# Kernel optimization log

Measured on AMD Instinct MI355X. Metric: run time of the kernel, lower is better.

Reference implementation:

```python
import jax, jax.numpy as jnp
import numpy as np

BS, L, D = 2048, 32, 768
KS = 5  # gaussian kernel size
EPS = 1e-5


def layer_norm(x, g, b):
    m = x.mean(-1, keepdims=True)
    var = ((x - m) ** 2).mean(-1, keepdims=True)
    return (x - m) * jax.lax.rsqrt(var + EPS) * g + b


def setup_inputs() -> dict:
    key = jax.random.key(0)
    ks = jax.random.split(key, 12)
    s = 0.02
    return {
        "v": jax.random.normal(ks[0], (BS, L, D), jnp.float32),
        "qa": jax.random.normal(ks[1], (BS, D), jnp.float32),
        # v_proj: LayerNorm -> Linear(D,D) -> GELU
        "vp_lng": jnp.ones((D,), jnp.float32),
        "vp_lnb": jnp.zeros((D,), jnp.float32),
        "vp_w": jax.random.normal(ks[2], (D, D), jnp.float32) * s,
        "vp_b": jnp.zeros((D,), jnp.float32),
        # qa_proj: LayerNorm -> Linear(D,D) -> GELU
        "qp_lng": jnp.ones((D,), jnp.float32),
        "qp_lnb": jnp.zeros((D,), jnp.float32),
        "qp_w": jax.random.normal(ks[3], (D, D), jnp.float32) * s,
        "qp_b": jnp.zeros((D,), jnp.float32),
        # grounding: LayerNorm -> Linear(D,D/2) -> GELU -> Linear(D/2,1) -> Softmax(dim=-2)
        "g_lng": jnp.ones((D,), jnp.float32),
        "g_lnb": jnp.zeros((D,), jnp.float32),
        "g_w1": jax.random.normal(ks[4], (D, D // 2), jnp.float32) * s,
        "g_b1": jnp.zeros((D // 2,), jnp.float32),
        "g_w2": jax.random.normal(ks[5], (D // 2, 1), jnp.float32) * s,
        "g_b2": jnp.zeros((1,), jnp.float32),
        # adaptive gaussian filter sigma (scalar parameter, initial 1.0)
        "sigma": jnp.array(1.0, jnp.float32),
    }


def reference(v, qa, vp_lng, vp_lnb, vp_w, vp_b, qp_lng, qp_lnb, qp_w, qp_b,
              g_lng, g_lnb, g_w1, g_b1, g_w2, g_b2, sigma):
    bs, length = v.shape[0], v.shape[1]
    # projections (exact erf GELU, matching torch nn.GELU default)
    v_p = jax.nn.gelu(layer_norm(v, vp_lng, vp_lnb) @ vp_w + vp_b, approximate=False)
    qa_p = jax.nn.gelu(layer_norm(qa, qp_lng, qp_lnb) @ qp_w + qp_b, approximate=False)
    # gate = tanh(v @ qa) : [bs, L, 1]
    gate = jnp.tanh(jnp.einsum('bld,bd->bl', v_p, qa_p))[..., None]
    # grounding head -> softmax over frames
    h = layer_norm(v_p * gate, g_lng, g_lnb)
    h = jax.nn.gelu(h @ g_w1 + g_b1, approximate=False)
    logits = h @ g_w2 + g_b2                      # [bs, L, 1]
    ori_key = jax.nn.softmax(logits, axis=1)[..., 0]  # [bs, L]
    # adaptive gaussian smoothing (depthwise conv1d, symmetric 5-tap kernel) + softmax
    xk = jnp.arange(KS, dtype=jnp.float32) - KS // 2
    kern = jnp.exp(-0.5 * (xk / sigma) ** 2)
    kern = kern / kern.sum()
    xp = jnp.pad(ori_key, ((0, 0), (KS // 2, KS // 2)))
    taps = jnp.stack([xp[:, k:k + length] for k in range(KS)], axis=0)  # [KS, bs, L]
    smoothed = jnp.einsum('k,kbl->bl', kern, taps)
    key_gs = jax.nn.softmax(smoothed, axis=1)         # [bs, L]
    # find_best_interval_v2, vectorized: among windows of size {1,3,5} that
    # contain the (first) argmax frame, pick the window with highest prob-sum;
    # ties resolve to smallest window then earliest start (strict > in loop ==
    # first occurrence of the max in (w, start) order == jnp.argmax semantics).
    pmax = jnp.argmax(key_gs, axis=1)                 # [bs]
    cum = jnp.pad(jnp.cumsum(key_gs, axis=1), ((0, 0), (1, 0)))
    scores_all, starts_all, ends_all = [], [], []
    for w in (1, 3, 5):
        s = jnp.arange(length - w + 1)
        sums = cum[:, s + w] - cum[:, s]              # sliding window sums
        contains = (pmax[:, None] >= s[None, :]) & (pmax[:, None] < s[None, :] + w)
        scores_all.append(jnp.where(contains, sums, -jnp.inf))
        starts_all.append(s)
        ends_all.append(s + w)                        # NOTE: exclusive end stored, as in original
    scores = jnp.concatenate(scores_all, axis=1)
    starts = jnp.concatenate(starts_all)
    ends = jnp.concatenate(ends_all)
    idx = jnp.argmax(scores, axis=1)
    st = starts[idx]
    en = ends[idx]
    max_indices = jnp.stack([st, en], axis=1)         # [bs, 2]
    rng = jnp.arange(length)
    mask = (rng[None, :] >= st[:, None]) & (rng[None, :] <= en[:, None])
    start_time = st.astype(jnp.float32) / 31.0
    end_time = en.astype(jnp.float32) / 31.0
    return key_gs, max_indices, start_time, end_time, mask, ori_key
```

## Files before the change

### kernel.cpp

```cpp
#include <hip/hip_runtime.h>
#include <math.h>
#include <stdint.h>


#define DEV __device__ __forceinline__

typedef __attribute__((ext_vector_type(8))) short short8v;
typedef __attribute__((ext_vector_type(4))) float f32x4;
typedef __attribute__((ext_vector_type(4))) uint32_t u32x4;

constexpr int KDIM  = 768;
constexpr int CHUNK = 32768;

constexpr int OFF_KG   = 0;
constexpr int OFF_MI   = 65536;
constexpr int OFF_ST   = 69632;
constexpr int OFF_ET   = 71680;
constexpr int OFF_MASK = 73728;
constexpr int OFF_ORI  = 139264;

DEV float wave_sum(float v) { for (int o = 32; o; o >>= 1) v += __shfl_xor(v, o); return v; }
DEV float wave_max(float v) { for (int o = 32; o; o >>= 1) v = fmaxf(v, __shfl_xor(v, o)); return v; }

DEV float gelu_fast(float x) {
    float z = x * 0.70710678118654752f;
    float s = fabsf(z);
    float t = __builtin_amdgcn_rcpf(fmaf(0.3275911f, s, 1.0f));
    float p = t * fmaf(t, fmaf(t, fmaf(t, fmaf(t, 1.061405429f, -1.453152027f),
                                       1.421413741f), -0.284496736f), 0.254829592f);
    float e = __expf(-s * s);
    float er = copysignf(1.0f - p * e, z);
    return 0.5f * x * (1.0f + er);
}

DEV short f2bf(float x) {
    uint32_t u = __builtin_bit_cast(uint32_t, x);
    u = u + 0x7fffu + ((u >> 16) & 1u);
    return (short)(u >> 16);
}
DEV float bf2f(short b) {
    uint32_t u = ((uint32_t)(uint16_t)b) << 16;
    return __builtin_bit_cast(float, u);
}
DEV float asf(uint32_t u) { return __builtin_bit_cast(float, u); }

DEV uint32_t packhl(float x) {
    uint32_t u  = __builtin_bit_cast(uint32_t, x);
    uint32_t hb = u & 0xffff0000u;
    float rem   = x - asf(hb);
    return hb | (uint32_t)(uint16_t)f2bf(rem);
}

DEV void gl_lds16(const void* g, void* l) {
    __builtin_amdgcn_global_load_lds(
        (const __attribute__((address_space(1))) uint32_t*)g,
        (__attribute__((address_space(3))) uint32_t*)l, 16, 0, 0);
}

DEV void unpack8(u32x4 p0, u32x4 p1, short8v& hi, short8v& lo) {
    u32x4 h, l;
    h.x = (p0.x >> 16) | (p0.y & 0xffff0000u);
    h.y = (p0.z >> 16) | (p0.w & 0xffff0000u);
    h.z = (p1.x >> 16) | (p1.y & 0xffff0000u);
    h.w = (p1.z >> 16) | (p1.w & 0xffff0000u);
    l.x = (p0.x & 0xffffu) | (p0.y << 16);
    l.y = (p0.z & 0xffffu) | (p0.w << 16);
    l.z = (p1.x & 0xffffu) | (p1.y << 16);
    l.w = (p1.z & 0xffffu) | (p1.w << 16);
    hi = __builtin_bit_cast(short8v, h);
    lo = __builtin_bit_cast(short8v, l);
}

__global__ __launch_bounds__(256)
void prep_A1(const float* __restrict__ X, const float* __restrict__ g,
             const float* __restrict__ b, short* __restrict__ Ah, short* __restrict__ Al)
{
    int w = threadIdx.x >> 6, lane = threadIdx.x & 63;
    int row = blockIdx.x * 4 + w;
    const float4* xr = (const float4*)(X + (size_t)row * KDIM);
    float4 xv[3]; float s = 0.f, ss = 0.f;
#pragma unroll
    for (int i = 0; i < 3; ++i) {
        xv[i] = xr[lane + i * 64];
        s  += xv[i].x + xv[i].y + xv[i].z + xv[i].w;
        ss += xv[i].x * xv[i].x + xv[i].y * xv[i].y + xv[i].z * xv[i].z + xv[i].w * xv[i].w;
    }
    s = wave_sum(s); ss = wave_sum(ss);
    float m = s * (1.f / 768.f), var = ss * (1.f / 768.f) - m * m;
    float sa = rsqrtf(var + 1e-5f), ta = -m * sa;
#pragma unroll
    for (int i = 0; i < 3; ++i) {
        int idx = lane + i * 64;
        float4 gv = ((const float4*)g)[idx];
        float4 bv = ((const float4*)b)[idx];
        float a0 = fmaf(fmaf(xv[i].x, sa, ta), gv.x, bv.x);
        float a1 = fmaf(fmaf(xv[i].y, sa, ta), gv.y, bv.y);
        float a2 = fmaf(fmaf(xv[i].z, sa, ta), gv.z, bv.z);
        float a3 = fmaf(fmaf(xv[i].w, sa, ta), gv.w, bv.w);
        short h0 = f2bf(a0), h1 = f2bf(a1), h2 = f2bf(a2), h3 = f2bf(a3);
        ushort4 hv, lv;
        hv.x = (uint16_t)h0; hv.y = (uint16_t)h1; hv.z = (uint16_t)h2; hv.w = (uint16_t)h3;
        lv.x = (uint16_t)f2bf(a0 - bf2f(h0)); lv.y = (uint16_t)f2bf(a1 - bf2f(h1));
        lv.z = (uint16_t)f2bf(a2 - bf2f(h2)); lv.w = (uint16_t)f2bf(a3 - bf2f(h3));
        ((ushort4*)(Ah + (size_t)row * KDIM))[idx] = hv;
        ((ushort4*)(Al + (size_t)row * KDIM))[idx] = lv;
    }
}

__global__ __launch_bounds__(256)
void prep_W(const float* __restrict__ W, const float* __restrict__ scale,
            short* __restrict__ Bh, short* __restrict__ Bl, int N)
{
    __shared__ float t[32][33];
    int bx = blockIdx.x, by = blockIdx.y;
    int lx = threadIdx.x & 31, ly = threadIdx.x >> 5;
#pragma unroll
    for (int r = 0; r < 32; r += 8)
        t[ly + r][lx] = W[(size_t)(by * 32 + ly + r) * N + bx * 32 + lx];
    __syncthreads();
    float sc = scale ? scale[by * 32 + lx] : 1.0f;
#pragma unroll
    for (int r = 0; r < 32; r += 8) {
        float v = t[lx][ly + r] * sc;
        short hi = f2bf(v);
        size_t o = (size_t)(bx * 32 + ly + r) * KDIM + by * 32 + lx;
        Bh[o] = hi;
        Bl[o] = f2bf(v - bf2f(hi));
    }
}

__global__ __launch_bounds__(256)
void colsums(const float* __restrict__ W1, const float* __restrict__ g2,
             const float* __restrict__ lb2, const float* __restrict__ b1,
             float* __restrict__ c1, float* __restrict__ c2)
{
    int w = threadIdx.x >> 6, lane = threadIdx.x & 63;
    int n = blockIdx.x * 4 + w;
    float s1 = 0.f, s2 = 0.f;
    for (int k = lane; k < 768; k += 64) {
        float wv = W1[(size_t)k * 384 + n];
        s1 += g2[k] * wv;
        s2 += lb2[k] * wv;
    }
    s1 = wave_sum(s1); s2 = wave_sum(s2);
    if (lane == 0) { c1[n] = s1; c2[n] = b1[n] + s2; }
}

__global__ __launch_bounds__(256)
void stats2(const float* __restrict__ sums, float2* __restrict__ st2, int chunk_off)
{
    int r = chunk_off + blockIdx.x * 256 + threadIdx.x;
    float s = 0.f, ss = 0.f, d = 0.f;
#pragma unroll
    for (int p = 0; p < 8; ++p) {
        s  += sums[(size_t)(0 * 8 + p) * 65536 + r];
        ss += sums[(size_t)(1 * 8 + p) * 65536 + r];
        d  += sums[(size_t)(2 * 8 + p) * 65536 + r];
    }
    float gate = tanhf(d);
    float m = s * (1.f / 768.f), var = ss * (1.f / 768.f) - m * m;
    float den = rsqrtf(gate * gate * var + 1e-5f);
    st2[r] = make_float2(gate * den, -gate * m * den);
}

#define VMW(N_) asm volatile("s_waitcnt vmcnt(" #N_ ")" ::: "memory")
#define SCB __builtin_amdgcn_sched_barrier(0)

#define STG(U_, KT_, KS_) gl_lds16(sp[U_] + (size_t)(KT_) * (KS_),            \
    lds + (((KT_) & 1) ? BUFSZ : 0) + (U_) * 4096 + toff)

#define STGALL(KT_) do {                                                      \
    STG(0, KT_, KSTA); STG(1, KT_, KSTA); STG(2, KT_, KSTA);                  \
    STG(3, KT_, KSTA); STG(4, KT_, 64); STG(5, KT_, 64); STG(6, KT_, 64);     \
    STG(7, KT_, 64); STG(8, KT_, 64); STG(9, KT_, 64); } while (0)

#define RDA(dst, BOFF) do { _Pragma("unroll")                                 \
    for (int mf = 0; mf < 4; ++mf) {                                          \
        int rA = wm * 64 + mf * 16 + lr;                                      \
        dst[mf] = *(const short8v*)(bb + (BOFF) + rA * 64 +                   \
                                    ((lh ^ ((rA >> 1) & 3)) << 4));           \
    } } while (0)

#define RDA2 do { RDA(ah, 0); RDA(al, 8192); } while (0)

#define RDAP do { _Pragma("unroll")                                           \
    for (int mf = 0; mf < 4; ++mf) {                                          \
        int rA = wm * 64 + mf * 16 + lr;                                      \
        const char* pr = bb + rA * 128;                                       \
        int x_ = rA & 7;                                                      \
        u32x4 p0 = *(const u32x4*)(pr + (((2 * lh) ^ x_) << 4));              \
        u32x4 p1 = *(const u32x4*)(pr + (((2 * lh + 1) ^ x_) << 4));          \
        unpack8(p0, p1, ah[mf], al[mf]);                                      \
    } } while (0)

#define RDB(dst, BOFF) do { _Pragma("unroll")                                 \
    for (int nf = 0; nf < 6; ++nf) {                                          \
        int rB = wn * 96 + nf * 16 + lr;                                      \
        dst[nf] = *(const short8v*)(bb + (BOFF) + rB * 64 +                   \
                                    ((lh ^ ((rB >> 1) & 3)) << 4));           \
    } } while (0)

#define BODY(KT_, NL_, ARD) do {                                              \
    if (NL_) { STGALL((KT_) + 1); }                                           \
    SCB;                                                                      \
    if (NL_) { VMW(10); } else { VMW(0); }                                    \
    SCB;                                                                      \
    __builtin_amdgcn_s_barrier();                \
    const char* bb = lds + (((KT_) & 1) ? BUFSZ : 0);                         \
    ARD; RDB(bh, 16384); RDB(bl, 28672);                                      \
    asm volatile("s_waitcnt lgkmcnt(0)" ::: "memory");                        \
    SCB;                                                                      \
    __builtin_amdgcn_s_barrier();                     \
    __builtin_amdgcn_s_setprio(1);                                            \
    _Pragma("unroll")                                                         \
    for (int mf = 0; mf < 4; ++mf)                                            \
        _Pragma("unroll")                                                     \
        for (int nf = 0; nf < 6; ++nf) {                                      \
            acc[mf][nf] = __builtin_amdgcn_mfma_f32_16x16x32_bf16(            \
                ah[mf], bh[nf], acc[mf][nf], 0, 0, 0);                        \
            acc[mf][nf] = __builtin_amdgcn_mfma_f32_16x16x32_bf16(            \
                ah[mf], bl[nf], acc[mf][nf], 0, 0, 0);                        \
            acc[mf][nf] = __builtin_amdgcn_mfma_f32_16x16x32_bf16(            \
                al[mf], bh[nf], acc[mf][nf], 0, 0, 0);                        \
        }                                                                     \
    __builtin_amdgcn_s_setprio(0);                                            \
    SCB;                                                                      \
} while (0)

template<int MODE>
__global__ __launch_bounds__(256, 2)
void gemm8(const short* __restrict__ Ah_g, const short* __restrict__ Al_g,
           const uint32_t* __restrict__ Ap_g,
           const short* __restrict__ Bh_g, const short* __restrict__ Bl_g,
           const float* __restrict__ bias, uint32_t* __restrict__ O_hl,
           const float* __restrict__ qa_p, float* __restrict__ sums,
           const float2* __restrict__ st2, const float* __restrict__ c1,
           const float* __restrict__ c2, const float* __restrict__ w2,
           float* __restrict__ partials, int chunk_off)
{
    constexpr int BUFSZ = 40960;
    constexpr int KSTA  = (MODE == 0) ? 64 : 128;
    extern __shared__ __align__(16) char lds[];

    const int t = threadIdx.x;
    const int w = t >> 6, lane = t & 63;
    const int lr = lane & 15, lh = lane >> 4;
    const int wm = w >> 1, wn = w & 1;

    const int gx = gridDim.x, nwg = gx * gridDim.y;
    int bidx = blockIdx.y * gx + blockIdx.x;
    int wid = (bidx & 7) * (nwg >> 3) + (bidx >> 3);
    const int bx = wid % gx, by = wid / gx;
    const int row0 = by * 128, col0 = bx * 192;

    const int r_ = t >> 2, c_ = t & 3;
    const int swz_ = (c_ ^ ((r_ >> 1) & 3)) << 3;
    const int rA_ = t >> 3, cA_ = t & 7;
    const int toff = t * 16;
    const char* sp[10];
    if (MODE == 0) {
        sp[0] = (const char*)(Ah_g + (size_t)(row0 + r_)      * KDIM + swz_);
        sp[1] = (const char*)(Ah_g + (size_t)(row0 + 64 + r_) * KDIM + swz_);
        sp[2] = (const char*)(Al_g + (size_t)(row0 + r_)      * KDIM + swz_);
        sp[3] = (const char*)(Al_g + (size_t)(row0 + 64 + r_) * KDIM + swz_);
    } else {
#pragma unroll
        for (int u = 0; u < 4; ++u)
            sp[u] = (const char*)(Ap_g + (size_t)(row0 + u * 32 + rA_) * KDIM
                                       + ((cA_ ^ (rA_ & 7)) << 2));
    }
    sp[4] = (const char*)(Bh_g + (size_t)(col0 + r_)       * KDIM + swz_);
    sp[5] = (const char*)(Bh_g + (size_t)(col0 + 64 + r_)  * KDIM + swz_);
    sp[6] = (const char*)(Bh_g + (size_t)(col0 + 128 + r_) * KDIM + swz_);
    sp[7] = (const char*)(Bl_g + (size_t)(col0 + r_)       * KDIM + swz_);
    sp[8] = (const char*)(Bl_g + (size_t)(col0 + 64 + r_)  * KDIM + swz_);
    sp[9] = (const char*)(Bl_g + (size_t)(col0 + 128 + r_) * KDIM + swz_);

    f32x4 acc[4][6] = {};
    short8v ah[4], al[4], bh[6], bl[6];

    STGALL(0);
    SCB;

    if (MODE == 0) {
        for (int kt = 0; kt < 24; kt += 2) {
            BODY(kt,     true,           RDA2);
            BODY(kt + 1, (kt + 1 < 23),  RDA2);
        }
    } else {
        for (int kt = 0; kt < 24; kt += 2) {
            BODY(kt,     true,           RDAP);
            BODY(kt + 1, (kt + 1 < 23),  RDAP);
        }
    }

    if (MODE == 0) {
        __syncthreads();
        float* qal = (float*)lds;
#pragma unroll
        for (int rr = 0; rr < 4; ++rr) {
            int bbase = (chunk_off >> 5) + (row0 >> 5);
            if (t < 192)
                qal[rr * 192 + t] = qa_p[(size_t)(bbase + rr) * 768 + col0 + t];
        }
        __syncthreads();

        float p[16][3];
#pragma unroll
        for (int mf = 0; mf < 4; ++mf) {
            const int bp = wm * 2 + (mf >> 1);
#pragma unroll
            for (int q = 0; q < 4; ++q) {
                int m = row0 + wm * 64 + mf * 16 + lh * 4 + q;
                float s = 0.f, ssq = 0.f, d = 0.f;
#pragma unroll
                for (int nf = 0; nf < 6; ++nf) {
                    int ncol = wn * 96 + nf * 16 + lr;
                    int n = col0 + ncol;
                    float gv = gelu_fast(acc[mf][nf][q] + bias[n]);
                    O_hl[(size_t)m * 768 + n] = packhl(gv);
                    s += gv; ssq += gv * gv; d += gv * qal[bp * 192 + ncol];
                }
                p[mf * 4 + q][0] = s; p[mf * 4 + q][1] = ssq; p[mf * 4 + q][2] = d;
            }
        }

        float r8[8][3], r4[4][3], r2[2][3], r1[3];
#pragma unroll
        for (int j = 0; j < 8; ++j)
#pragma unroll
            for (int v = 0; v < 3; ++v) {
                float e = p[2 * j][v]     + __shfl_xor(p[2 * j][v], 1);
                float o = p[2 * j + 1][v] + __shfl_xor(p[2 * j + 1][v], 1);
                r8[j][v] = (lr & 1) ? o : e;
            }
#pragma unroll
        for (int j = 0; j < 4; ++j)
#pragma unroll
            for (int v = 0; v < 3; ++v) {
                float e = r8[2 * j][v]     + __shfl_xor(r8[2 * j][v], 2);
                float o = r8[2 * j + 1][v] + __shfl_xor(r8[2 * j + 1][v], 2);
                r4[j][v] = (lr & 2) ? o : e;
            }
#pragma unroll
        for (int j = 0; j < 2; ++j)
#pragma unroll
            for (int v = 0; v < 3; ++v) {
                float e = r4[2 * j][v]     + __shfl_xor(r4[2 * j][v], 4);
                float o = r4[2 * j + 1][v] + __shfl_xor(r4[2 * j + 1][v], 4);
                r2[j][v] = (lr & 4) ? o : e;
            }
#pragma unroll
        for (int v = 0; v < 3; ++v) {
            float e = r2[0][v] + __shfl_xor(r2[0][v], 8);
            float o = r2[1][v] + __shfl_xor(r2[1][v], 8);
            r1[v] = (lr & 8) ? o : e;
        }

        {
            int gr = chunk_off + row0 + wm * 64 + (lr >> 2) * 16 + lh * 4 + (lr & 3);
            int pc = bx * 2 + wn;
            sums[(size_t)(0 * 8 + pc) * 65536 + gr] = r1[0];
            sums[(size_t)(1 * 8 + pc) * 65536 + gr] = r1[1];
            sums[(size_t)(2 * 8 + pc) * 65536 + gr] = r1[2];
        }
    } else {
        float c1v[6], c2v[6], wv[6];
#pragma unroll
        for (int nf = 0; nf < 6; ++nf) {
            int n = col0 + wn * 96 + nf * 16 + lr;
            c1v[nf] = c1[n]; c2v[nf] = c2[n]; wv[nf] = w2[n];
        }
        float rs[4][4] = {};
#pragma unroll
        for (int mf = 0; mf < 4; ++mf)
#pragma unroll
            for (int q = 0; q < 4; ++q) {
                int gm = chunk_off + row0 + wm * 64 + mf * 16 + lh * 4 + q;
                float2 st = st2[gm];
#pragma unroll
                for (int nf = 0; nf < 6; ++nf) {
                    float h = fmaf(st.x, acc[mf][nf][q], fmaf(st.y, c1v[nf], c2v[nf]));
                    rs[mf][q] += gelu_fast(h) * wv[nf];
                }
            }
#pragma unroll
        for (int mf = 0; mf < 4; ++mf)
#pragma unroll
            for (int q = 0; q < 4; ++q) {
                float vv = rs[mf][q];
                vv += __shfl_xor(vv, 1); vv += __shfl_xor(vv, 2);
                vv += __shfl_xor(vv, 4); vv += __shfl_xor(vv, 8);
                if (lr == 0) {
                    int gm = chunk_off + row0 + wm * 64 + mf * 16 + lh * 4 + q;
                    partials[(size_t)(bx * 2 + wn) * 65536 + gm] = vv;
                }
            }
    }
}

constexpr int BKF = 16;
__global__ __launch_bounds__(256)
void rowstats(const float* __restrict__ X, float2* __restrict__ st, int M)
{
    int wave = threadIdx.x >> 6, lane = threadIdx.x & 63;
    int row = blockIdx.x * 4 + wave;
    if (row >= M) return;
    const float4* xr = reinterpret_cast<const float4*>(X + (size_t)row * KDIM);
    float s = 0.f, ss = 0.f;
#pragma unroll
    for (int i = 0; i < 3; ++i) {
        float4 v = xr[lane + i * 64];
        s  += v.x + v.y + v.z + v.w;
        ss += v.x * v.x + v.y * v.y + v.z * v.z + v.w * v.w;
    }
    s = wave_sum(s); ss = wave_sum(ss);
    if (lane == 0) {
        float m = s * (1.0f / 768.0f);
        float var = ss * (1.0f / 768.0f) - m * m;
        float rstd = rsqrtf(var + 1e-5f);
        st[row] = make_float2(rstd, -m * rstd);
    }
}

template<int BM, int BN, int TM, int TN>
__global__ __launch_bounds__(256)
void gemm_fused(const float* __restrict__ X, const float2* __restrict__ st,
                const float* __restrict__ gw, const float* __restrict__ gb,
                const float* __restrict__ W, const float* __restrict__ bias,
                float* __restrict__ out, int M, int N)
{
    static_assert((BM / TM) * (BN / TN) == 256, "256 threads");
    __shared__ float As[BKF][BM];
    __shared__ float Bs[BKF][BN];
    const int t = threadIdx.x;
    constexpr int TXN = BN / TN;
    const int tx = t % TXN;
    const int ty = t / TXN;
    const int row0 = blockIdx.y * BM;
    const int col0 = blockIdx.x * BN;
    float acc[TM][TN] = {};
    constexpr int A_IT = BM * BKF / 4 / 256;
    constexpr int B_IT = BKF * BN / 4 / 256;
    for (int k0 = 0; k0 < KDIM; k0 += BKF) {
#pragma unroll
        for (int i = 0; i < A_IT; ++i) {
            int idx = t + i * 256;
            int r = idx >> 2;
            int c = (idx & 3) << 2;
            float4 xv = *reinterpret_cast<const float4*>(X + (size_t)(row0 + r) * KDIM + k0 + c);
            float2 s = st[row0 + r];
            float4 gv = *reinterpret_cast<const float4*>(gw + k0 + c);
            float4 bv = *reinterpret_cast<const float4*>(gb + k0 + c);
            As[c + 0][r] = fmaf(fmaf(xv.x, s.x, s.y), gv.x, bv.x);
            As[c + 1][r] = fmaf(fmaf(xv.y, s.x, s.y), gv.y, bv.y);
            As[c + 2][r] = fmaf(fmaf(xv.z, s.x, s.y), gv.z, bv.z);
            As[c + 3][r] = fmaf(fmaf(xv.w, s.x, s.y), gv.w, bv.w);
        }
#pragma unroll
        for (int i = 0; i < B_IT; ++i) {
            int idx = t + i * 256;
            int r = idx / (BN / 4);
            int c = (idx % (BN / 4)) << 2;
            *reinterpret_cast<float4*>(&Bs[r][c]) =
                *reinterpret_cast<const float4*>(W + (size_t)(k0 + r) * N + col0 + c);
        }
        __syncthreads();
#pragma unroll
        for (int kk = 0; kk < BKF; ++kk) {
            float a[TM], b[TN];
#pragma unroll
            for (int i = 0; i < TM; i += 4)
                *reinterpret_cast<float4*>(&a[i]) = *reinterpret_cast<const float4*>(&As[kk][ty * TM + i]);
#pragma unroll
            for (int j = 0; j < TN; j += 4)
                *reinterpret_cast<float4*>(&b[j]) = *reinterpret_cast<const float4*>(&Bs[kk][tx * TN + j]);
#pragma unroll
            for (int i = 0; i < TM; ++i)
#pragma unroll
                for (int j = 0; j < TN; ++j)
                    acc[i][j] = fmaf(a[i], b[j], acc[i][j]);
        }
        __syncthreads();
    }
#pragma unroll
    for (int i = 0; i < TM; ++i) {
        size_t row = row0 + ty * TM + i;
#pragma unroll
        for (int j = 0; j < TN; j += 4) {
            int col = col0 + tx * TN + j;
            float4 o;
            o.x = gelu_fast(acc[i][j + 0] + bias[col + 0]);
            o.y = gelu_fast(acc[i][j + 1] + bias[col + 1]);
            o.z = gelu_fast(acc[i][j + 2] + bias[col + 2]);
            o.w = gelu_fast(acc[i][j + 3] + bias[col + 3]);
            *reinterpret_cast<float4*>(out + row * N + col) = o;
        }
    }
}

__global__ __launch_bounds__(64)
void head_kernel(const float* __restrict__ partials, const float* __restrict__ b2,
                 const float* __restrict__ sigma_p, float* __restrict__ out)
{
    int b = blockIdx.x, lane = threadIdx.x;
    __shared__ float ok[36];
    __shared__ float kg[32];
    __shared__ int sel[2];

    if (lane < 36) ok[lane] = 0.f;
    __syncthreads();

    float x = -3.4e38f;
    if (lane < 32) {
        int row = b * 32 + lane;
        x = b2[0];
#pragma unroll
        for (int p = 0; p < 4; ++p) x += partials[(size_t)p * 65536 + row];
    }
    float mx = wave_max(x);
    float e = (lane < 32) ? expf(x - mx) : 0.f;
    float sum = wave_sum(e);
    float ori = e / sum;
    if (lane < 32) {
        out[OFF_ORI + b * 32 + lane] = ori;
        ok[lane + 2] = ori;
    }
    __syncthreads();

    float sg = sigma_p[0];
    float kern[5]; float ks = 0.f;
#pragma unroll
    for (int k = 0; k < 5; ++k) { float xx = (float)(k - 2) / sg; kern[k] = expf(-0.5f * xx * xx); ks += kern[k]; }
    float sm = -3.4e38f;
    if (lane < 32) {
        sm = 0.f;
#pragma unroll
        for (int k = 0; k < 5; ++k) sm += (kern[k] / ks) * ok[lane + k];
    }
    float mx2 = wave_max(sm);
    float e2 = (lane < 32) ? expf(sm - mx2) : 0.f;
    float sum2 = wave_sum(e2);
    float kgv = e2 / sum2;
    if (lane < 32) {
        out[OFF_KG + b * 32 + lane] = kgv;
        kg[lane] = kgv;
    }
    __syncthreads();

    if (lane == 0) {
        int pm = 0; float bv = kg[0];
        for (int i = 1; i < 32; ++i) if (kg[i] > bv) { bv = kg[i]; pm = i; }
        float cum[33]; cum[0] = 0.f;
        for (int i = 0; i < 32; ++i) cum[i + 1] = cum[i] + kg[i];
        float bs = -3.4e38f; int bst = 0, ben = 0;
        const int wsz[3] = {1, 3, 5};
        for (int wi = 0; wi < 3; ++wi) {
            int w = wsz[wi];
            for (int s = 0; s + w <= 32; ++s) {
                if (pm >= s && pm < s + w) {
                    float sc = cum[s + w] - cum[s];
                    if (sc > bs) { bs = sc; bst = s; ben = s + w; }
                }
            }
        }
        out[OFF_MI + b * 2 + 0] = (float)bst;
        out[OFF_MI + b * 2 + 1] = (float)ben;
        out[OFF_ST + b] = (float)bst / 31.0f;
        out[OFF_ET + b] = (float)ben / 31.0f;
        sel[0] = bst; sel[1] = ben;
    }
    __syncthreads();
    if (lane < 32)
        out[OFF_MASK + b * 32 + lane] = (lane >= sel[0] && lane <= sel[1]) ? 1.0f : 0.0f;
}

extern "C" void kernel_launch(void* const* d_in, const int* in_sizes, int n_in,
                              void* d_out, int out_size, void* d_ws, size_t ws_size,
                              hipStream_t stream)
{
    const float* v      = (const float*)d_in[0];
    const float* qa     = (const float*)d_in[1];
    const float* vp_lng = (const float*)d_in[2];
    const float* vp_lnb = (const float*)d_in[3];
    const float* vp_w   = (const float*)d_in[4];
    const float* vp_b   = (const float*)d_in[5];
    const float* qp_lng = (const float*)d_in[6];
    const float* qp_lnb = (const float*)d_in[7];
    const float* qp_w   = (const float*)d_in[8];
    const float* qp_b   = (const float*)d_in[9];
    const float* g_lng  = (const float*)d_in[10];
    const float* g_lnb  = (const float*)d_in[11];
    const float* g_w1   = (const float*)d_in[12];
    const float* g_b1   = (const float*)d_in[13];
    const float* g_w2   = (const float*)d_in[14];
    const float* g_b2   = (const float*)d_in[15];
    const float* sigma  = (const float*)d_in[16];
    float* outf = (float*)d_out;

    short* A1h = (short*)d_ws;
    short* A1l = A1h + (size_t)CHUNK * KDIM;
    uint32_t* vp_hl = (uint32_t*)(A1l + (size_t)CHUNK * KDIM);
    short* B1h = (short*)(vp_hl + (size_t)CHUNK * KDIM);
    short* B1l = B1h + 768 * KDIM;
    short* B2h = B1l + 768 * KDIM;
    short* B2l = B2h + 384 * KDIM;
    float* qa_p = (float*)(B2l + 384 * KDIM);
    float* st_qa = qa_p + 2048 * KDIM;
    float* partials = st_qa + 4096;
    float* sums = partials + 4 * 65536;
    float2* st2 = (float2*)(sums + 24 * 65536);
    float* c1 = (float*)(st2 + 65536);
    float* c2 = c1 + 384;

    rowstats<<<512, 256, 0, stream>>>(qa, (float2*)st_qa, 2048);
    gemm_fused<64, 64, 4, 4><<<dim3(12, 32), 256, 0, stream>>>(
        qa, (const float2*)st_qa, qp_lng, qp_lnb, qp_w, qp_b, qa_p, 2048, 768);

    prep_W<<<dim3(24, 24), 256, 0, stream>>>(vp_w, nullptr, B1h, B1l, 768);
    prep_W<<<dim3(12, 24), 256, 0, stream>>>(g_w1, g_lng, B2h, B2l, 384);
    colsums<<<96, 256, 0, stream>>>(g_w1, g_lng, g_lnb, g_b1, c1, c2);

    constexpr int LDS8 = 81920;

    for (int c = 0; c < 65536; c += CHUNK) {
        prep_A1<<<CHUNK / 4, 256, 0, stream>>>(v + (size_t)c * KDIM, vp_lng, vp_lnb, A1h, A1l);
        gemm8<0><<<dim3(4, CHUNK / 128), 256, LDS8, stream>>>(
            A1h, A1l, nullptr, B1h, B1l, vp_b, vp_hl, qa_p, sums,
            nullptr, nullptr, nullptr, nullptr, nullptr, c);
        stats2<<<CHUNK / 256, 256, 0, stream>>>(sums, st2, c);
        gemm8<1><<<dim3(2, CHUNK / 128), 256, LDS8, stream>>>(
            nullptr, nullptr, vp_hl, B2h, B2l, nullptr, nullptr, nullptr, nullptr,
            (const float2*)st2, c1, c2, g_w2, partials, c);
    }

    head_kernel<<<2048, 64, 0, stream>>>(partials, g_b2, sigma, outf);
}
```

Measured before the change: 497.2 us.

## Fuse LayerNorm hi/lo split into GEMM A-tile load, fold gamma/beta into weights

Removes the prep_A1 pass, which wrote bf16 hi/lo copies of the normalized input. The first GEMM now streams raw fp32 v rows into LDS and applies per-row mean/rstd while splitting into hi/lo fragments in registers. LayerNorm gamma is folded into the weight conversion, and beta into a precomputed bias via a new column-sum kernel. This trades a full read and write of the A operand for extra ALU work inside the GEMM inner loop. Hi is now truncated rather than rounded, which may slightly change numerics.

```diff
diff --git a/kernel.cpp b/kernel.cpp
--- a/kernel.cpp
+++ b/kernel.cpp
@@ -49,6 +49,21 @@
     uint32_t hb = u & 0xffff0000u;
     float rem   = x - asf(hb);
     return hb | (uint32_t)(uint16_t)f2bf(rem);
+}
+
+struct HL { uint32_t hi, lo; };
+DEV HL ln_split_pair(float x0, float x1, float sa, float ta) {
+    float a0 = fmaf(x0, sa, ta), a1 = fmaf(x1, sa, ta);
+    uint32_t u0 = __builtin_bit_cast(uint32_t, a0);
+    uint32_t u1 = __builtin_bit_cast(uint32_t, a1);
+    uint32_t h0 = u0 & 0xffff0000u, h1 = u1 & 0xffff0000u;
+    float r0 = a0 - asf(h0), r1 = a1 - asf(h1);
+    uint32_t v0 = __builtin_bit_cast(uint32_t, r0);
+    uint32_t v1 = __builtin_bit_cast(uint32_t, r1);
+    HL out;
+    out.hi = (h0 >> 16) | h1;
+    out.lo = (v0 >> 16) | (v1 & 0xffff0000u);
+    return out;
 }
 
 DEV void gl_lds16(const void* g, void* l) {
@@ -72,42 +87,6 @@
 }
 
 __global__ __launch_bounds__(256)
-void prep_A1(const float* __restrict__ X, const float* __restrict__ g,
-             const float* __restrict__ b, short* __restrict__ Ah, short* __restrict__ Al)
-{
-    int w = threadIdx.x >> 6, lane = threadIdx.x & 63;
-    int row = blockIdx.x * 4 + w;
-    const float4* xr = (const float4*)(X + (size_t)row * KDIM);
-    float4 xv[3]; float s = 0.f, ss = 0.f;
-#pragma unroll
-    for (int i = 0; i < 3; ++i) {
-        xv[i] = xr[lane + i * 64];
-        s  += xv[i].x + xv[i].y + xv[i].z + xv[i].w;
-        ss += xv[i].x * xv[i].x + xv[i].y * xv[i].y + xv[i].z * xv[i].z + xv[i].w * xv[i].w;
-    }
-    s = wave_sum(s); ss = wave_sum(ss);
-    float m = s * (1.f / 768.f), var = ss * (1.f / 768.f) - m * m;
-    float sa = rsqrtf(var + 1e-5f), ta = -m * sa;
-#pragma unroll
-    for (int i = 0; i < 3; ++i) {
-        int idx = lane + i * 64;
-        float4 gv = ((const float4*)g)[idx];
-        float4 bv = ((const float4*)b)[idx];
-        float a0 = fmaf(fmaf(xv[i].x, sa, ta), gv.x, bv.x);
-        float a1 = fmaf(fmaf(xv[i].y, sa, ta), gv.y, bv.y);
-        float a2 = fmaf(fmaf(xv[i].z, sa, ta), gv.z, bv.z);
-        float a3 = fmaf(fmaf(xv[i].w, sa, ta), gv.w, bv.w);
-        short h0 = f2bf(a0), h1 = f2bf(a1), h2 = f2bf(a2), h3 = f2bf(a3);
-        ushort4 hv, lv;
-        hv.x = (uint16_t)h0; hv.y = (uint16_t)h1; hv.z = (uint16_t)h2; hv.w = (uint16_t)h3;
-        lv.x = (uint16_t)f2bf(a0 - bf2f(h0)); lv.y = (uint16_t)f2bf(a1 - bf2f(h1));
-        lv.z = (uint16_t)f2bf(a2 - bf2f(h2)); lv.w = (uint16_t)f2bf(a3 - bf2f(h3));
-        ((ushort4*)(Ah + (size_t)row * KDIM))[idx] = hv;
-        ((ushort4*)(Al + (size_t)row * KDIM))[idx] = lv;
-    }
-}
-
-__global__ __launch_bounds__(256)
 void prep_W(const float* __restrict__ W, const float* __restrict__ scale,
             short* __restrict__ Bh, short* __restrict__ Bl, int N)
 {
@@ -147,6 +126,19 @@
 }
 
 __global__ __launch_bounds__(256)
+void colsums768(const float* __restrict__ W, const float* __restrict__ lb,
+                const float* __restrict__ bias, float* __restrict__ outb)
+{
+    int w = threadIdx.x >> 6, lane = threadIdx.x & 63;
+    int n = blockIdx.x * 4 + w;
+    float s = 0.f;
+    for (int k = lane; k < 768; k += 64)
+        s += lb[k] * W[(size_t)k * 768 + n];
+    s = wave_sum(s);
+    if (lane == 0) outb[n] = bias[n] + s;
+}
+
+__global__ __launch_bounds__(256)
 void stats2(const float* __restrict__ sums, float2* __restrict__ st2, int chunk_off)
 {
     int r = chunk_off + blockIdx.x * 256 + threadIdx.x;
@@ -163,6 +155,29 @@
     st2[r] = make_float2(gate * den, -gate * m * den);
 }
 
+__global__ __launch_bounds__(256)
+void rowstats(const float* __restrict__ X, float2* __restrict__ st, int M)
+{
+    int wave = threadIdx.x >> 6, lane = threadIdx.x & 63;
+    int row = blockIdx.x * 4 + wave;
+    if (row >= M) return;
+    const float4* xr = reinterpret_cast<const float4*>(X + (size_t)row * KDIM);
+    float s = 0.f, ss = 0.f;
+#pragma unroll
+    for (int i = 0; i < 3; ++i) {
+        float4 v = xr[lane + i * 64];
+        s  += v.x + v.y + v.z + v.w;
+        ss += v.x * v.x + v.y * v.y + v.z * v.z + v.w * v.w;
+    }
+    s = wave_sum(s); ss = wave_sum(ss);
+    if (lane == 0) {
+        float m = s * (1.0f / 768.0f);
+        float var = ss * (1.0f / 768.0f) - m * m;
+        float rstd = rsqrtf(var + 1e-5f);
+        st[row] = make_float2(rstd, -m * rstd);
+    }
+}
+
 #define VMW(N_) asm volatile("s_waitcnt vmcnt(" #N_ ")" ::: "memory")
 #define SCB __builtin_amdgcn_sched_barrier(0)
 
@@ -170,18 +185,27 @@
     lds + (((KT_) & 1) ? BUFSZ : 0) + (U_) * 4096 + toff)
 
 #define STGALL(KT_) do {                                                      \
-    STG(0, KT_, KSTA); STG(1, KT_, KSTA); STG(2, KT_, KSTA);                  \
-    STG(3, KT_, KSTA); STG(4, KT_, 64); STG(5, KT_, 64); STG(6, KT_, 64);     \
+    STG(0, KT_, 128); STG(1, KT_, 128); STG(2, KT_, 128);                     \
+    STG(3, KT_, 128); STG(4, KT_, 64); STG(5, KT_, 64); STG(6, KT_, 64);      \
     STG(7, KT_, 64); STG(8, KT_, 64); STG(9, KT_, 64); } while (0)
 
-#define RDA(dst, BOFF) do { _Pragma("unroll")                                 \
+#define RDAF do { _Pragma("unroll")                                           \
     for (int mf = 0; mf < 4; ++mf) {                                          \
         int rA = wm * 64 + mf * 16 + lr;                                      \
-        dst[mf] = *(const short8v*)(bb + (BOFF) + rA * 64 +                   \
-                                    ((lh ^ ((rA >> 1) & 3)) << 4));           \
+        const char* pr = bb + rA * 128;                                       \
+        int x_ = rA & 7;                                                      \
+        f32x4 v0 = *(const f32x4*)(pr + (((2 * lh) ^ x_) << 4));              \
+        f32x4 v1 = *(const f32x4*)(pr + (((2 * lh + 1) ^ x_) << 4));          \
+        HL q0 = ln_split_pair(v0.x, v0.y, stv[mf].x, stv[mf].y);              \
+        HL q1 = ln_split_pair(v0.z, v0.w, stv[mf].x, stv[mf].y);              \
+        HL q2 = ln_split_pair(v1.x, v1.y, stv[mf].x, stv[mf].y);              \
+        HL q3 = ln_split_pair(v1.z, v1.w, stv[mf].x, stv[mf].y);              \
+        u32x4 hh, ll;                                                         \
+        hh.x = q0.hi; hh.y = q1.hi; hh.z = q2.hi; hh.w = q3.hi;               \
+        ll.x = q0.lo; ll.y = q1.lo; ll.z = q2.lo; ll.w = q3.lo;               \
+        ah[mf] = __builtin_bit_cast(short8v, hh);                             \
+        al[mf] = __builtin_bit_cast(short8v, ll);                             \
     } } while (0)
-
-#define RDA2 do { RDA(ah, 0); RDA(al, 8192); } while (0)
 
 #define RDAP do { _Pragma("unroll")                                           \
     for (int mf = 0; mf < 4; ++mf) {                                          \
@@ -229,7 +253,7 @@
 
 template<int MODE>
 __global__ __launch_bounds__(256, 2)
-void gemm8(const short* __restrict__ Ah_g, const short* __restrict__ Al_g,
+void gemm8(const float* __restrict__ Av_g, const float2* __restrict__ stv_g,
            const uint32_t* __restrict__ Ap_g,
            const short* __restrict__ Bh_g, const short* __restrict__ Bl_g,
            const float* __restrict__ bias, uint32_t* __restrict__ O_hl,
@@ -239,7 +263,6 @@
            float* __restrict__ partials, int chunk_off)
 {
     constexpr int BUFSZ = 40960;
-    constexpr int KSTA  = (MODE == 0) ? 64 : 128;
     extern __shared__ __align__(16) char lds[];
 
     const int t = threadIdx.x;
@@ -252,6 +275,13 @@
     int wid = (bidx & 7) * (nwg >> 3) + (bidx >> 3);
     const int bx = wid % gx, by = wid / gx;
     const int row0 = by * 128, col0 = bx * 192;
+
+    float2 stv[4];
+    if (MODE == 0) {
+#pragma unroll
+        for (int mf = 0; mf < 4; ++mf)
+            stv[mf] = stv_g[row0 + wm * 64 + mf * 16 + lr];
+    }
 
     const int r_ = t >> 2, c_ = t & 3;
     const int swz_ = (c_ ^ ((r_ >> 1) & 3)) << 3;
@@ -259,10 +289,10 @@
     const int toff = t * 16;
     const char* sp[10];
     if (MODE == 0) {
-        sp[0] = (const char*)(Ah_g + (size_t)(row0 + r_)      * KDIM + swz_);
-        sp[1] = (const char*)(Ah_g + (size_t)(row0 + 64 + r_) * KDIM + swz_);
-        sp[2] = (const char*)(Al_g + (size_t)(row0 + r_)      * KDIM + swz_);
-        sp[3] = (const char*)(Al_g + (size_t)(row0 + 64 + r_) * KDIM + swz_);
+#pragma unroll
+        for (int u = 0; u < 4; ++u)
+            sp[u] = (const char*)(Av_g + (size_t)(row0 + u * 32 + rA_) * KDIM
+                                       + ((cA_ ^ (rA_ & 7)) << 2));
     } else {
 #pragma unroll
         for (int u = 0; u < 4; ++u)
@@ -284,8 +314,8 @@
 
     if (MODE == 0) {
         for (int kt = 0; kt < 24; kt += 2) {
-            BODY(kt,     true,           RDA2);
-            BODY(kt + 1, (kt + 1 < 23),  RDA2);
+            BODY(kt,     true,           RDAF);
+            BODY(kt + 1, (kt + 1 < 23),  RDAF);
         }
     } else {
         for (int kt = 0; kt < 24; kt += 2) {
@@ -400,29 +430,6 @@
 }
 
 constexpr int BKF = 16;
-__global__ __launch_bounds__(256)
-void rowstats(const float* __restrict__ X, float2* __restrict__ st, int M)
-{
-    int wave = threadIdx.x >> 6, lane = threadIdx.x & 63;
-    int row = blockIdx.x * 4 + wave;
-    if (row >= M) return;
-    const float4* xr = reinterpret_cast<const float4*>(X + (size_t)row * KDIM);
-    float s = 0.f, ss = 0.f;
-#pragma unroll
-    for (int i = 0; i < 3; ++i) {
-        float4 v = xr[lane + i * 64];
-        s  += v.x + v.y + v.z + v.w;
-        ss += v.x * v.x + v.y * v.y + v.z * v.z + v.w * v.w;
-    }
-    s = wave_sum(s); ss = wave_sum(ss);
-    if (lane == 0) {
-        float m = s * (1.0f / 768.0f);
-        float var = ss * (1.0f / 768.0f) - m * m;
-        float rstd = rsqrtf(var + 1e-5f);
-        st[row] = make_float2(rstd, -m * rstd);
-    }
-}
-
 template<int BM, int BN, int TM, int TN>
 __global__ __launch_bounds__(256)
 void gemm_fused(const float* __restrict__ X, const float2* __restrict__ st,
@@ -598,9 +605,7 @@
     const float* sigma  = (const float*)d_in[16];
     float* outf = (float*)d_out;
 
-    short* A1h = (short*)d_ws;
-    short* A1l = A1h + (size_t)CHUNK * KDIM;
-    uint32_t* vp_hl = (uint32_t*)(A1l + (size_t)CHUNK * KDIM);
+    uint32_t* vp_hl = (uint32_t*)d_ws;
     short* B1h = (short*)(vp_hl + (size_t)CHUNK * KDIM);
     short* B1l = B1h + 768 * KDIM;
     short* B2h = B1l + 768 * KDIM;
@@ -612,21 +617,25 @@
     float2* st2 = (float2*)(sums + 24 * 65536);
     float* c1 = (float*)(st2 + 65536);
     float* c2 = c1 + 384;
+    float* bias1v = c2 + 384;
+    float2* st_v = (float2*)(bias1v + 768);
 
     rowstats<<<512, 256, 0, stream>>>(qa, (float2*)st_qa, 2048);
     gemm_fused<64, 64, 4, 4><<<dim3(12, 32), 256, 0, stream>>>(
         qa, (const float2*)st_qa, qp_lng, qp_lnb, qp_w, qp_b, qa_p, 2048, 768);
 
-    prep_W<<<dim3(24, 24), 256, 0, stream>>>(vp_w, nullptr, B1h, B1l, 768);
+    prep_W<<<dim3(24, 24), 256, 0, stream>>>(vp_w, vp_lng, B1h, B1l, 768);
     prep_W<<<dim3(12, 24), 256, 0, stream>>>(g_w1, g_lng, B2h, B2l, 384);
+    colsums768<<<192, 256, 0, stream>>>(vp_w, vp_lnb, vp_b, bias1v);
     colsums<<<96, 256, 0, stream>>>(g_w1, g_lng, g_lnb, g_b1, c1, c2);
 
     constexpr int LDS8 = 81920;
 
     for (int c = 0; c < 65536; c += CHUNK) {
-        prep_A1<<<CHUNK / 4, 256, 0, stream>>>(v + (size_t)c * KDIM, vp_lng, vp_lnb, A1h, A1l);
+        rowstats<<<CHUNK / 4, 256, 0, stream>>>(v + (size_t)c * KDIM, st_v, CHUNK);
         gemm8<0><<<dim3(4, CHUNK / 128), 256, LDS8, stream>>>(
-            A1h, A1l, nullptr, B1h, B1l, vp_b, vp_hl, qa_p, sums,
+            v + (size_t)c * KDIM, (const float2*)st_v, nullptr, B1h, B1l,
+            bias1v, vp_hl, qa_p, sums,
             nullptr, nullptr, nullptr, nullptr, nullptr, c);
         stats2<<<CHUNK / 256, 256, 0, stream>>>(sums, st2, c);
         gemm8<1><<<dim3(2, CHUNK / 128), 256, LDS8, stream>>>(
```

Result: no change. 506.2 us (+1.8%).
